# Optimization experiments

Hardware: AMD Instinct MI355X
Metric: run time of the kernel (lower is better)

Reference implementation:

```python
import jax, jax.numpy as jnp
import numpy as np

ROUTINGS = 3
NUM_CAPSULES = 16


def squash(s, eps=1e-8):
    # s: [..., dim_capsule]
    norm = jnp.linalg.norm(s, axis=-1, keepdims=True)
    return (norm ** 2) / (1.0 + norm ** 2) * (s / (norm + eps))


def setup_inputs() -> dict:
    key = jax.random.key(0)
    k1, k2 = jax.random.split(key)
    x = jax.random.normal(k1, (64, 1024, 64), dtype=jnp.float32)      # [B, n_in, input_dim]
    weight = jax.random.normal(k2, (16, 64, 32), dtype=jnp.float32)    # [nc, input_dim, dc]
    return {"x": x, "weight": weight}


def reference(x, weight):
    B, n_in, _ = x.shape
    nc = weight.shape[0]
    # prediction vectors u_hat: [B, nc, n_in, dc]
    u_hat = jnp.einsum('bni,cid->bcnd', x, weight)
    # routing logits, softmax taken over the output-capsule axis (dim=1 in torch)
    b = jnp.zeros((B, nc, n_in, 1), dtype=u_hat.dtype)
    v = None
    for i in range(ROUTINGS):
        c = jax.nn.softmax(b, axis=1)                 # [B, nc, n_in, 1]
        s = jnp.sum(c * u_hat, axis=2)                # [B, nc, dc]
        v = squash(s)                                 # [B, nc, dc]
        if i < ROUTINGS - 1:
            # agreement: <u_hat, v> per input capsule
            b = b + jnp.einsum('bcnd,bcd->bcn', u_hat, v)[..., None]
    return v
```

## Files before the change

kernel.cpp:

```cpp
#include <hip/hip_runtime.h>
#include <math.h>

#define B_SZ 64
#define N_IN 1024
#define IDIM 64
#define NC   16
#define DC   32
#define NQ   4
#define QR   256
#define NTHR 1024
#define XS   68
#define AS   20

#define WS_CNT 0
#define WS_CS  1024
#define WS_SP1 17408
#define WS_SP2 279552
#define WS_WV0 541696

__device__ __forceinline__ void st_agent(float* p, float v) {
    __hip_atomic_store(p, v, __ATOMIC_RELAXED, __HIP_MEMORY_SCOPE_AGENT);
}
__device__ __forceinline__ float ld_agent(const float* p) {
    return __hip_atomic_load(p, __ATOMIC_RELAXED, __HIP_MEMORY_SCOPE_AGENT);
}
__device__ __forceinline__ float rdlane_f(float v, int l) {
    return __int_as_float(__builtin_amdgcn_readlane(__float_as_int(v), l));
}

__global__ __launch_bounds__(1024) void k_reset(int* cnt) {
    __hip_atomic_store(&cnt[threadIdx.x], 0, __ATOMIC_RELAXED, __HIP_MEMORY_SCOPE_AGENT);
}


__device__ __forceinline__ void stage_x(const float* __restrict__ x, float* xT,
                                        int b, int q, int tid) {
    const float4* xb4 = reinterpret_cast<const float4*>(x + ((size_t)b * N_IN + q * QR) * IDIM);
#pragma unroll
    for (int m = 0; m < 4; m++) {
        const int f = tid + m * NTHR;
        const float4 v4 = xb4[f];
        const int n = f >> 4, i0 = (f & 15) * 4;
        *reinterpret_cast<float4*>(&xT[n * XS + i0]) = v4;
    }
}

__device__ __forceinline__ float route_pass(const float* xT, const float* wSm,
                                            float* aSmT, float* pSm,
                                            int tid, int lane, int wave,
                                            int row, int grp, int rq) {
    const float4 wr4 = *reinterpret_cast<const float4*>(&wSm[lane * AS + grp * 4]);
    {
        float a0 = 0.f, a1 = 0.f, a2 = 0.f, a3 = 0.f;
#pragma unroll
        for (int iq = 0; iq < 16; iq++) {
            const float4 xv = *reinterpret_cast<const float4*>(&xT[row * XS + iq * 4]);
#pragma unroll
            for (int j = 0; j < 4; j++) {
                const int i = iq * 4 + j;
                const float xc = (j == 0) ? xv.x : (j == 1) ? xv.y
                               : (j == 2) ? xv.z : xv.w;
                a0 += rdlane_f(wr4.x, i) * xc;
                a1 += rdlane_f(wr4.y, i) * xc;
                a2 += rdlane_f(wr4.z, i) * xc;
                a3 += rdlane_f(wr4.w, i) * xc;
            }
        }
        *reinterpret_cast<float4*>(&aSmT[row * AS + grp * 4]) =
            make_float4(a0, a1, a2, a3);
    }
    __syncthreads();
    float cw0, cw1, cw2, cw3;
    {
        const float4 q0 = *reinterpret_cast<const float4*>(&aSmT[row * AS + 0]);
        const float4 q1 = *reinterpret_cast<const float4*>(&aSmT[row * AS + 4]);
        const float4 q2 = *reinterpret_cast<const float4*>(&aSmT[row * AS + 8]);
        const float4 q3 = *reinterpret_cast<const float4*>(&aSmT[row * AS + 12]);
        float av[NC] = {q0.x, q0.y, q0.z, q0.w, q1.x, q1.y, q1.z, q1.w,
                        q2.x, q2.y, q2.z, q2.w, q3.x, q3.y, q3.z, q3.w};
        float mx = av[0];
#pragma unroll
        for (int k = 1; k < NC; k++) mx = fmaxf(mx, av[k]);
        float ss = 0.f;
#pragma unroll
        for (int k = 0; k < NC; k++) { av[k] = __expf(av[k] - mx); ss += av[k]; }
        const float inv = 1.f / ss;
        if (grp == 0)      { cw0 = av[0];  cw1 = av[1];  cw2 = av[2];  cw3 = av[3];  }
        else if (grp == 1) { cw0 = av[4];  cw1 = av[5];  cw2 = av[6];  cw3 = av[7];  }
        else if (grp == 2) { cw0 = av[8];  cw1 = av[9];  cw2 = av[10]; cw3 = av[11]; }
        else               { cw0 = av[12]; cw1 = av[13]; cw2 = av[14]; cw3 = av[15]; }
        cw0 *= inv; cw1 *= inv; cw2 *= inv; cw3 *= inv;
    }
    {
        float s0 = 0.f, s1 = 0.f, s2 = 0.f, s3 = 0.f;
#pragma unroll
        for (int nl = 0; nl < 64; nl++) {
            const float xv = xT[(rq * 64 + nl) * XS + lane];
            s0 += rdlane_f(cw0, nl) * xv;
            s1 += rdlane_f(cw1, nl) * xv;
            s2 += rdlane_f(cw2, nl) * xv;
            s3 += rdlane_f(cw3, nl) * xv;
        }
        *reinterpret_cast<float4*>(&pSm[(rq * 64 + lane) * AS + grp * 4]) =
            make_float4(s0, s1, s2, s3);
    }
    __syncthreads();
    return pSm[(0 * 64 + lane) * AS + wave] + pSm[(1 * 64 + lane) * AS + wave] +
           pSm[(2 * 64 + lane) * AS + wave] + pSm[(3 * 64 + lane) * AS + wave];
}

__device__ __forceinline__ void caps_sv(const float* __restrict__ W, const float* redSm,
                                        float* vSm, int tid, bool modeRed0, bool toOut,
                                        float* __restrict__ outp, int b, int q) {
    if (tid < 512) {
        const int c = tid >> 5, dd = tid & 31;
        const float* Wc = W + c * (IDIM * DC) + dd;
        float s = 0.f;
#pragma unroll 8
        for (int i = 0; i < IDIM; i++) {
            const float rv = modeRed0 ? redSm[i] : redSm[c * 64 + i];
            s += rv * Wc[i * DC];
        }
        if (modeRed0) s *= 0.0625f;
        float n2 = s * s;
#pragma unroll
        for (int m = 16; m >= 1; m >>= 1) n2 += __shfl_xor(n2, m);
        const float g = (n2 / (1.f + n2)) / (sqrtf(n2) + 1e-8f);
        if (toOut) { if (q == 0) outp[b * (NC * DC) + c * DC + dd] = g * s; }
        else       vSm[c * 36 + dd] = g * s;
    }
    __syncthreads();
}

__device__ __forceinline__ float caps_wv(const float* __restrict__ W, const float* vSm,
                                         int tid) {
    const int i = tid >> 4, c = tid & 15;
    const float4* Wr = reinterpret_cast<const float4*>(W + (size_t)(c * IDIM + i) * DC);
    const float4* vv = reinterpret_cast<const float4*>(&vSm[c * 36]);
    float acc = 0.f;
#pragma unroll
    for (int dq = 0; dq < 8; dq++) {
        const float4 wq = Wr[dq], vq = vv[dq];
        acc += wq.x * vq.x + wq.y * vq.y + wq.z * vq.z + wq.w * vq.w;
    }
    return acc;
}

__global__ __launch_bounds__(NTHR, 1)
void k_phase1(const float* __restrict__ x, const float* __restrict__ W,
              int* __restrict__ cnt, float* __restrict__ cs,
              float* __restrict__ sp1, float* __restrict__ wv0) {
    const int b = blockIdx.x & 63, q = blockIdx.x >> 6;
    const int tid = threadIdx.x, lane = tid & 63, wave = tid >> 6;
    const int row = tid & 255, grp = tid >> 8, rq = wave & 3;

    __shared__ float __align__(16) xT[QR * XS];
    __shared__ float __align__(16) aSmT[QR * AS];
    __shared__ float __align__(16) pSm[4 * 64 * AS];
    __shared__ float __align__(16) wSm[IDIM * AS];
    __shared__ float redSm[NC * IDIM];
    __shared__ float __align__(16) vSm[NC * 36];

    stage_x(x, xT, b, q, tid);
    __syncthreads();

    {
        float s = 0.f;
#pragma unroll
        for (int t = 0; t < 16; t++) s += xT[(wave * 16 + t) * XS + lane];
        redSm[wave * 64 + lane] = s;
    }
    __syncthreads();
    if (tid < 64) {
        float r = 0.f;
#pragma unroll
        for (int w2 = 0; w2 < 16; w2++) r += redSm[w2 * 64 + tid];
        st_agent(&cs[(b * NQ + q) * 64 + tid], r);
    }
    __syncthreads();
    if (tid == 0)
        __hip_atomic_fetch_add(&cnt[b * 16], 1, __ATOMIC_RELEASE, __HIP_MEMORY_SCOPE_AGENT);
    if (tid == 0)
        while (__hip_atomic_load(&cnt[b * 16], __ATOMIC_ACQUIRE,
                                 __HIP_MEMORY_SCOPE_AGENT) < NQ)
            __builtin_amdgcn_s_sleep(1);
    __syncthreads();
    if (tid < 64) {
        float r = 0.f;
#pragma unroll
        for (int k = 0; k < NQ; k++) r += ld_agent(&cs[(b * NQ + k) * 64 + tid]);
        redSm[tid] = r;
    }
    __syncthreads();

    caps_sv(W, redSm, vSm, tid, true, false, nullptr, b, q);
    {
        const float acc = caps_wv(W, vSm, tid);
        wSm[(tid >> 4) * AS + (tid & 15)] = acc;
        if (q == 0) wv0[b * 1024 + tid] = acc;
    }
    __syncthreads();

    const float val = route_pass(xT, wSm, aSmT, pSm, tid, lane, wave, row, grp, rq);
    sp1[(size_t)(b * NQ + q) * 1024 + tid] = val;
}

__global__ __launch_bounds__(NTHR, 1)
void k_phase2(const float* __restrict__ x, const float* __restrict__ W,
              float* __restrict__ out, int* __restrict__ cnt,
              const float* __restrict__ sp1, float* __restrict__ sp2,
              const float* __restrict__ wv0) {
    const int b = blockIdx.x & 63, q = blockIdx.x >> 6;
    const int tid = threadIdx.x, lane = tid & 63, wave = tid >> 6;
    const int row = tid & 255, grp = tid >> 8, rq = wave & 3;

    __shared__ float __align__(16) xT[QR * XS];
    __shared__ float __align__(16) aSmT[QR * AS];
    __shared__ float __align__(16) pSm[4 * 64 * AS];
    __shared__ float __align__(16) wSm[IDIM * AS];
    __shared__ float redSm[NC * IDIM];
    __shared__ float __align__(16) vSm[NC * 36];

    stage_x(x, xT, b, q, tid);
    {
        float r = 0.f;
#pragma unroll
        for (int k = 0; k < NQ; k++) r += sp1[(size_t)(b * NQ + k) * 1024 + tid];
        redSm[tid] = r;
    }
    __syncthreads();

    caps_sv(W, redSm, vSm, tid, false, false, nullptr, b, q);
    wSm[(tid >> 4) * AS + (tid & 15)] = caps_wv(W, vSm, tid) + wv0[b * 1024 + tid];
    __syncthreads();

    const float val = route_pass(xT, wSm, aSmT, pSm, tid, lane, wave, row, grp, rq);
    st_agent(&sp2[(size_t)(b * NQ + q) * 1024 + tid], val);

    __syncthreads();
    if (tid == 0)
        __hip_atomic_fetch_add(&cnt[b * 16], 1, __ATOMIC_RELEASE, __HIP_MEMORY_SCOPE_AGENT);
    if (q != 0) return;
    if (tid == 0)
        while (__hip_atomic_load(&cnt[b * 16], __ATOMIC_ACQUIRE,
                                 __HIP_MEMORY_SCOPE_AGENT) < 2 * NQ)
            __builtin_amdgcn_s_sleep(1);
    __syncthreads();
    {
        float r = val;
#pragma unroll
        for (int k = 1; k < NQ; k++) r += ld_agent(&sp2[(size_t)(b * NQ + k) * 1024 + tid]);
        redSm[tid] = r;
    }
    __syncthreads();
    caps_sv(W, redSm, vSm, tid, false, true, out, b, q);
}

extern "C" void kernel_launch(void* const* d_in, const int* in_sizes, int n_in,
                              void* d_out, int out_size, void* d_ws, size_t ws_size,
                              hipStream_t stream) {
    const float* x = (const float*)d_in[0];
    const float* W = (const float*)d_in[1];
    float* out = (float*)d_out;
    float* ws = (float*)d_ws;

    int*   cnt = (int*)(ws + WS_CNT);
    float* cs  = ws + WS_CS;
    float* sp1 = ws + WS_SP1;
    float* sp2 = ws + WS_SP2;
    float* wv0 = ws + WS_WV0;

    k_reset<<<1, 1024, 0, stream>>>(cnt);
    k_phase1<<<B_SZ * NQ, NTHR, 0, stream>>>(x, W, cnt, cs, sp1, wv0);
    k_phase2<<<B_SZ * NQ, NTHR, 0, stream>>>(x, W, out, cnt, sp1, sp2, wv0);
}
```

Before: 48.10 us.

## Replace in-kernel atomic spin barriers with separate colsum and final kernels

```diff
diff --git a/kernel.cpp b/kernel.cpp
--- a/kernel.cpp
+++ b/kernel.cpp
@@ -12,24 +12,13 @@
 #define XS   68
 #define AS   20
 
-#define WS_CNT 0
-#define WS_CS  1024
-#define WS_SP1 17408
-#define WS_SP2 279552
-#define WS_WV0 541696
-
-__device__ __forceinline__ void st_agent(float* p, float v) {
-    __hip_atomic_store(p, v, __ATOMIC_RELAXED, __HIP_MEMORY_SCOPE_AGENT);
-}
-__device__ __forceinline__ float ld_agent(const float* p) {
-    return __hip_atomic_load(p, __ATOMIC_RELAXED, __HIP_MEMORY_SCOPE_AGENT);
-}
+#define WS_CS  0
+#define WS_SP1 16384
+#define WS_SP2 278528
+#define WS_WV0 540672
+
 __device__ __forceinline__ float rdlane_f(float v, int l) {
     return __int_as_float(__builtin_amdgcn_readlane(__float_as_int(v), l));
-}
-
-__global__ __launch_bounds__(1024) void k_reset(int* cnt) {
-    __hip_atomic_store(&cnt[threadIdx.x], 0, __ATOMIC_RELAXED, __HIP_MEMORY_SCOPE_AGENT);
 }
 
 
@@ -111,7 +100,7 @@
 
 __device__ __forceinline__ void caps_sv(const float* __restrict__ W, const float* redSm,
                                         float* vSm, int tid, bool modeRed0, bool toOut,
-                                        float* __restrict__ outp, int b, int q) {
+                                        float* __restrict__ outp, int b) {
     if (tid < 512) {
         const int c = tid >> 5, dd = tid & 31;
         const float* Wc = W + c * (IDIM * DC) + dd;
@@ -126,7 +115,7 @@
 #pragma unroll
         for (int m = 16; m >= 1; m >>= 1) n2 += __shfl_xor(n2, m);
         const float g = (n2 / (1.f + n2)) / (sqrtf(n2) + 1e-8f);
-        if (toOut) { if (q == 0) outp[b * (NC * DC) + c * DC + dd] = g * s; }
+        if (toOut) outp[b * (NC * DC) + c * DC + dd] = g * s;
         else       vSm[c * 36 + dd] = g * s;
     }
     __syncthreads();
@@ -146,10 +135,34 @@
     return acc;
 }
 
+__global__ __launch_bounds__(256) void k_colsum(const float* __restrict__ x,
+                                                float* __restrict__ cs) {
+    const int b = blockIdx.y, q = blockIdx.x;
+    const int tid = threadIdx.x;
+    const float4* xb4 = reinterpret_cast<const float4*>(x + ((size_t)b * N_IN + q * QR) * IDIM);
+    float4 s4 = {0.f, 0.f, 0.f, 0.f};
+#pragma unroll
+    for (int m = 0; m < 16; m++) {
+        const float4 v4 = xb4[tid + m * 256];
+        s4.x += v4.x; s4.y += v4.y; s4.z += v4.z; s4.w += v4.w;
+    }
+    __shared__ float red[16][64];
+    const int g = tid >> 4, i0 = (tid & 15) * 4;
+    red[g][i0 + 0] = s4.x; red[g][i0 + 1] = s4.y;
+    red[g][i0 + 2] = s4.z; red[g][i0 + 3] = s4.w;
+    __syncthreads();
+    if (tid < 64) {
+        float r = 0.f;
+#pragma unroll
+        for (int k = 0; k < 16; k++) r += red[k][tid];
+        cs[(b * NQ + q) * 64 + tid] = r;
+    }
+}
+
 __global__ __launch_bounds__(NTHR, 1)
-void k_phase1(const float* __restrict__ x, const float* __restrict__ W,
-              int* __restrict__ cnt, float* __restrict__ cs,
-              float* __restrict__ sp1, float* __restrict__ wv0) {
+void k_iter1(const float* __restrict__ x, const float* __restrict__ W,
+             const float* __restrict__ cs, float* __restrict__ sp1,
+             float* __restrict__ wv0) {
     const int b = blockIdx.x & 63, q = blockIdx.x >> 6;
     const int tid = threadIdx.x, lane = tid & 63, wave = tid >> 6;
     const int row = tid & 255, grp = tid >> 8, rq = wave & 3;
@@ -162,54 +175,28 @@
     __shared__ float __align__(16) vSm[NC * 36];
 
     stage_x(x, xT, b, q, tid);
-    __syncthreads();
-
-    {
-        float s = 0.f;
-#pragma unroll
-        for (int t = 0; t < 16; t++) s += xT[(wave * 16 + t) * XS + lane];
-        redSm[wave * 64 + lane] = s;
-    }
-    __syncthreads();
     if (tid < 64) {
         float r = 0.f;
 #pragma unroll
-        for (int w2 = 0; w2 < 16; w2++) r += redSm[w2 * 64 + tid];
-        st_agent(&cs[(b * NQ + q) * 64 + tid], r);
-    }
-    __syncthreads();
-    if (tid == 0)
-        __hip_atomic_fetch_add(&cnt[b * 16], 1, __ATOMIC_RELEASE, __HIP_MEMORY_SCOPE_AGENT);
-    if (tid == 0)
-        while (__hip_atomic_load(&cnt[b * 16], __ATOMIC_ACQUIRE,
-                                 __HIP_MEMORY_SCOPE_AGENT) < NQ)
-            __builtin_amdgcn_s_sleep(1);
-    __syncthreads();
-    if (tid < 64) {
-        float r = 0.f;
-#pragma unroll
-        for (int k = 0; k < NQ; k++) r += ld_agent(&cs[(b * NQ + k) * 64 + tid]);
+        for (int k = 0; k < NQ; k++) r += cs[(b * NQ + k) * 64 + tid];
         redSm[tid] = r;
     }
     __syncthreads();
-
-    caps_sv(W, redSm, vSm, tid, true, false, nullptr, b, q);
+    caps_sv(W, redSm, vSm, tid, true, false, nullptr, b);
     {
         const float acc = caps_wv(W, vSm, tid);
         wSm[(tid >> 4) * AS + (tid & 15)] = acc;
         if (q == 0) wv0[b * 1024 + tid] = acc;
     }
     __syncthreads();
-
     const float val = route_pass(xT, wSm, aSmT, pSm, tid, lane, wave, row, grp, rq);
     sp1[(size_t)(b * NQ + q) * 1024 + tid] = val;
 }
 
 __global__ __launch_bounds__(NTHR, 1)
-void k_phase2(const float* __restrict__ x, const float* __restrict__ W,
-              float* __restrict__ out, int* __restrict__ cnt,
-              const float* __restrict__ sp1, float* __restrict__ sp2,
-              const float* __restrict__ wv0) {
+void k_iter2(const float* __restrict__ x, const float* __restrict__ W,
+             const float* __restrict__ sp1, float* __restrict__ sp2,
+             const float* __restrict__ wv0) {
     const int b = blockIdx.x & 63, q = blockIdx.x >> 6;
     const int tid = threadIdx.x, lane = tid & 63, wave = tid >> 6;
     const int row = tid & 255, grp = tid >> 8, rq = wave & 3;
@@ -229,31 +216,27 @@
         redSm[tid] = r;
     }
     __syncthreads();
-
-    caps_sv(W, redSm, vSm, tid, false, false, nullptr, b, q);
+    caps_sv(W, redSm, vSm, tid, false, false, nullptr, b);
     wSm[(tid >> 4) * AS + (tid & 15)] = caps_wv(W, vSm, tid) + wv0[b * 1024 + tid];
     __syncthreads();
-
     const float val = route_pass(xT, wSm, aSmT, pSm, tid, lane, wave, row, grp, rq);
-    st_agent(&sp2[(size_t)(b * NQ + q) * 1024 + tid], val);
-
-    __syncthreads();
-    if (tid == 0)
-        __hip_atomic_fetch_add(&cnt[b * 16], 1, __ATOMIC_RELEASE, __HIP_MEMORY_SCOPE_AGENT);
-    if (q != 0) return;
-    if (tid == 0)
-        while (__hip_atomic_load(&cnt[b * 16], __ATOMIC_ACQUIRE,
-                                 __HIP_MEMORY_SCOPE_AGENT) < 2 * NQ)
-            __builtin_amdgcn_s_sleep(1);
-    __syncthreads();
-    {
-        float r = val;
-#pragma unroll
-        for (int k = 1; k < NQ; k++) r += ld_agent(&sp2[(size_t)(b * NQ + k) * 1024 + tid]);
+    sp2[(size_t)(b * NQ + q) * 1024 + tid] = val;
+}
+
+__global__ __launch_bounds__(NTHR) void k_final(const float* __restrict__ sp2,
+                                                const float* __restrict__ W,
+                                                float* __restrict__ out) {
+    const int b = blockIdx.x, tid = threadIdx.x;
+    __shared__ float redSm[NC * IDIM];
+    __shared__ float __align__(16) vSm[NC * 36];
+    {
+        float r = 0.f;
+#pragma unroll
+        for (int k = 0; k < NQ; k++) r += sp2[(size_t)(b * NQ + k) * 1024 + tid];
         redSm[tid] = r;
     }
     __syncthreads();
-    caps_sv(W, redSm, vSm, tid, false, true, out, b, q);
+    caps_sv(W, redSm, vSm, tid, false, true, out, b);
 }
 
 extern "C" void kernel_launch(void* const* d_in, const int* in_sizes, int n_in,
@@ -264,13 +247,13 @@
     float* out = (float*)d_out;
     float* ws = (float*)d_ws;
 
-    int*   cnt = (int*)(ws + WS_CNT);
     float* cs  = ws + WS_CS;
     float* sp1 = ws + WS_SP1;
     float* sp2 = ws + WS_SP2;
     float* wv0 = ws + WS_WV0;
 
-    k_reset<<<1, 1024, 0, stream>>>(cnt);
-    k_phase1<<<B_SZ * NQ, NTHR, 0, stream>>>(x, W, cnt, cs, sp1, wv0);
-    k_phase2<<<B_SZ * NQ, NTHR, 0, stream>>>(x, W, out, cnt, sp1, sp2, wv0);
-}
+    k_colsum<<<dim3(NQ, B_SZ), 256, 0, stream>>>(x, cs);
+    k_iter1<<<B_SZ * NQ, NTHR, 0, stream>>>(x, W, cs, sp1, wv0);
+    k_iter2<<<B_SZ * NQ, NTHR, 0, stream>>>(x, W, sp1, sp2, wv0);
+    k_final<<<B_SZ, NTHR, 0, stream>>>(sp2, W, out);
+}
```

Measured after the change: 43.99 us. 1.09x faster.
